# Performance work log

Measured on AMD Instinct MI355X. Metric: run time of the kernel, lower is better.

The kernel has to match this reference:

```python
import jax, jax.numpy as jnp
import numpy as np

N = 50000
E = 640000
NFEAT = 128
NHID = 128
ALPHA = 0.2  # leaky relu slope


def setup_inputs() -> dict:
    key = jax.random.key(0)
    k1, k2, k3, k4, k5 = jax.random.split(key, 5)
    x = jax.random.normal(k1, (N, NFEAT), dtype=jnp.float32)
    W = jax.random.normal(k2, (NFEAT, NHID), dtype=jnp.float32) * (1.0 / np.sqrt(NFEAT))
    a = jax.random.normal(k3, (1, 2 * NHID), dtype=jnp.float32) * 0.1
    # every node appears at least once as a source so rowsum > 0 (as in a real adjacency)
    src = jnp.concatenate([jnp.arange(N, dtype=jnp.int64 if jax.config.read('jax_enable_x64') else jnp.int32),
                           jax.random.randint(k4, (E - N,), 0, N)]).astype(jnp.int32)
    dst = jax.random.randint(k5, (E,), 0, N).astype(jnp.int32)
    edge_index = jnp.stack([src, dst], axis=0)
    return {"x": x, "W": W, "a": a, "edge_index": edge_index, "no_need_param": 0}


def reference(x, W, a, edge_index, no_need_param):
    # SpGraphAttentionLayer (concat=False), single head
    h = x @ W                                   # [N, nhid]
    src, dst = edge_index[0], edge_index[1]     # [E]
    nhid = W.shape[1]
    a1, a2 = a[0, :nhid], a[0, nhid:]
    # a @ cat(h[src], h[dst])  ==  h[src]@a1 + h[dst]@a2
    score = h[src] @ a1 + h[dst] @ a2           # [E]
    e = jnp.exp(-jax.nn.leaky_relu(score, ALPHA))
    n = x.shape[0]
    rowsum = jax.ops.segment_sum(e, src, num_segments=n)              # [N]
    h_prime = jax.ops.segment_sum(e[:, None] * h[dst], src, num_segments=n)  # [N, nhid]
    neighborhood_emb = h_prime / (rowsum[:, None] + 1e-16)
    # fused combine: elu(x @ W - neighborhood aggregation)
    mapped_fea = x @ W
    return jax.nn.elu(mapped_fea - neighborhood_emb)
```

## Files before the change

### kernel.cpp

```cpp
#include <hip/hip_runtime.h>
#include <hip/hip_fp16.h>
#include <math.h>

#define NFEAT 128
#define NHID  128
#define ALPHA 0.2f

typedef __attribute__((ext_vector_type(8))) short short8;
typedef __attribute__((ext_vector_type(4))) float f32x4;

__device__ inline unsigned int pack_bf16x2_rn(float x, float y) {
    unsigned int bx = __float_as_uint(x), by = __float_as_uint(y);
    bx += 0x7fffu + ((bx >> 16) & 1u);
    by += 0x7fffu + ((by >> 16) & 1u);
    return (bx >> 16) | (by & 0xffff0000u);
}

union Frag { unsigned int u[4]; uint4 v; short8 s; };

__global__ __launch_bounds__(256) void prep_wt_kernel(
    const float* __restrict__ W, unsigned int* __restrict__ Wtg)
{
    __shared__ float tile[32][33];
    const int t  = threadIdx.x;
    const int kt = blockIdx.x >> 2;
    const int nt = blockIdx.x & 3;

    {
        const int r = t >> 3, c = t & 7;
        const float4 v = *((const float4*)&W[(size_t)(kt * 32 + r) * NHID + nt * 32 + c * 4]);
        tile[r][c * 4 + 0] = v.x; tile[r][c * 4 + 1] = v.y;
        tile[r][c * 4 + 2] = v.z; tile[r][c * 4 + 3] = v.w;
    }
    __syncthreads();

    const int nn = t & 31;
    #pragma unroll
    for (int i = 0; i < 2; ++i) {
        const int kk = (t >> 5) * 2 + i;
        Wtg[(size_t)(nt * 32 + nn) * 64 + kt * 16 + kk] =
            pack_bf16x2_rn(tile[kk * 2][nn], tile[kk * 2 + 1][nn]);
    }
}

__global__ __launch_bounds__(256) void gemm_h_kernel(
    const float* __restrict__ x, const unsigned int* __restrict__ Wtg,
    const float* __restrict__ a, float* __restrict__ h,
    unsigned int* __restrict__ hbu,
    float* __restrict__ s1, float* __restrict__ s2, int n,
    const int* __restrict__ ei, int* __restrict__ hist, int E)
{
    __shared__ unsigned int Wtu[128 * 68];

    const int t = threadIdx.x;

    #pragma unroll
    for (int i = 0; i < 8; ++i) {
        const int u  = i * 256 + t;
        const uint4 v = ((const uint4*)Wtg)[u];
        const int nn = u >> 4, kc = u & 15;
        *((uint4*)&Wtu[nn * 68 + kc * 4]) = v;
    }

    {
        const int E4   = E >> 2;
        const int nthr = gridDim.x << 8;
        const int g    = blockIdx.x * 256 + t;
        for (int idx = g; idx < E4; idx += nthr) {
            const int4 s4 = ((const int4*)ei)[idx];
            atomicAdd(&hist[s4.x], 1);
            atomicAdd(&hist[s4.y], 1);
            atomicAdd(&hist[s4.z], 1);
            atomicAdd(&hist[s4.w], 1);
        }
        for (int j = (E4 << 2) + g; j < E; j += nthr) atomicAdd(&hist[ei[j]], 1);
    }
    __syncthreads();

    const int w    = t >> 6;
    const int lane = t & 63;
    const int c    = lane & 15;
    const int quad = lane >> 4;

    const int rowbase = blockIdx.x * 128 + w * 32;

    float a1v[8], a2v[8];
    #pragma unroll
    for (int tt = 0; tt < 8; ++tt) {
        a1v[tt] = a[tt * 16 + c];
        a2v[tt] = a[NHID + tt * 16 + c];
    }

    f32x4 acc[2][8];
    #pragma unroll
    for (int rt = 0; rt < 2; ++rt)
        #pragma unroll
        for (int tt = 0; tt < 8; ++tt)
            acc[rt][tt] = (f32x4){0.f, 0.f, 0.f, 0.f};

    #pragma unroll
    for (int s = 0; s < 4; ++s) {
        Frag afr[2];
        #pragma unroll
        for (int rt = 0; rt < 2; ++rt) {
            int row = rowbase + rt * 16 + c;
            if (row >= n) row = n - 1;
            const float* xp = x + (size_t)row * NFEAT + s * 32 + quad * 8;
            const float4 xa = *((const float4*)xp);
            const float4 xb = *((const float4*)(xp + 4));
            afr[rt].u[0] = pack_bf16x2_rn(xa.x, xa.y);
            afr[rt].u[1] = pack_bf16x2_rn(xa.z, xa.w);
            afr[rt].u[2] = pack_bf16x2_rn(xb.x, xb.y);
            afr[rt].u[3] = pack_bf16x2_rn(xb.z, xb.w);
        }
        #pragma unroll
        for (int tt = 0; tt < 8; ++tt) {
            Frag bfr;
            bfr.v = *((const uint4*)&Wtu[(tt * 16 + c) * 68 + s * 16 + quad * 4]);
            acc[0][tt] = __builtin_amdgcn_mfma_f32_16x16x32_bf16(
                afr[0].s, bfr.s, acc[0][tt], 0, 0, 0);
            acc[1][tt] = __builtin_amdgcn_mfma_f32_16x16x32_bf16(
                afr[1].s, bfr.s, acc[1][tt], 0, 0, 0);
        }
    }

    #pragma unroll
    for (int rt = 0; rt < 2; ++rt) {
        #pragma unroll
        for (int r = 0; r < 4; ++r) {
            const int  row = rowbase + rt * 16 + quad * 4 + r;
            const bool ok  = (row < n);
            float p1 = 0.f, p2 = 0.f;
            #pragma unroll
            for (int tt = 0; tt < 8; ++tt) {
                const float v = acc[rt][tt][r];
                if (ok) h[(size_t)row * NHID + tt * 16 + c] = v;
                p1 = fmaf(v, a1v[tt], p1);
                p2 = fmaf(v, a2v[tt], p2);
            }
            #pragma unroll
            for (int p = 0; p < 4; ++p) {
                if (ok) hbu[(size_t)row * 64 + p * 16 + c] =
                    pack_bf16x2_rn(acc[rt][2 * p][r], acc[rt][2 * p + 1][r]);
            }
            #pragma unroll
            for (int off = 1; off <= 8; off <<= 1) {
                p1 += __shfl_xor(p1, off, 64);
                p2 += __shfl_xor(p2, off, 64);
            }
            if (ok && c == 0) { s1[row] = p1; s2[row] = p2; }
        }
    }
}

__global__ __launch_bounds__(256) void scan_block_kernel(
    const int* __restrict__ in, int* __restrict__ out, int* __restrict__ bsums, int n)
{
    __shared__ int s[256];
    const int tid = threadIdx.x;
    const int gid = blockIdx.x * 256 + tid;
    const int v = (gid < n) ? in[gid] : 0;
    s[tid] = v;
    __syncthreads();
    #pragma unroll
    for (int off = 1; off < 256; off <<= 1) {
        const int t2 = (tid >= off) ? s[tid - off] : 0;
        __syncthreads();
        s[tid] += t2;
        __syncthreads();
    }
    if (gid < n) out[gid] = s[tid] - v;
    if (tid == 255 && bsums) bsums[blockIdx.x] = s[255];
}

__global__ __launch_bounds__(256) void scan_add_kernel(
    int* __restrict__ row_ptr, int* __restrict__ cursor,
    const int* __restrict__ bsums_scan, int n, int E)
{
    const int gid = blockIdx.x * 256 + threadIdx.x;
    if (gid < n) {
        const int v = row_ptr[gid] + bsums_scan[gid >> 8];
        row_ptr[gid] = v;
        cursor[gid]  = v;
    }
    if (gid == 0) row_ptr[n] = E;
}

__global__ __launch_bounds__(256) void scatter_kernel(
    const int* __restrict__ ei, const float* __restrict__ s1,
    const float* __restrict__ s2, int* __restrict__ cursor,
    unsigned int* __restrict__ erec, int E)
{
    const int j = blockIdx.x * 256 + threadIdx.x;
    if (j >= E) return;
    const int src = ei[j];
    const int dst = ei[E + j];
    float s = s1[src] + s2[dst];
    s = (s > 0.f) ? s : ALPHA * s;
    const float ev = expf(-s);
    const unsigned int evh = (unsigned int)__half_as_ushort(__float2half(ev));
    const int pos = atomicAdd(&cursor[src], 1);
    erec[pos] = ((unsigned int)dst << 16) | evh;
}

__global__ __launch_bounds__(256) void aggregate_kernel(
    const int* __restrict__ row_ptr, const unsigned int* __restrict__ erec,
    const unsigned int* __restrict__ hbu, const float* __restrict__ h,
    float* __restrict__ out, int n)
{
    const int node = blockIdx.x * 16 + (threadIdx.x >> 4);
    const int l    = threadIdx.x & 15;
    if (node >= n) return;

    const int beg = row_ptr[node];
    const int end = row_ptr[node + 1];

    float acc[8];
    #pragma unroll
    for (int i = 0; i < 8; ++i) acc[i] = 0.f;
    float rs = 0.f;

    #define BL(x) __uint_as_float((x) << 16)
    #define BH(x) __uint_as_float((x) & 0xffff0000u)
    #define ACC4(u, ev)                                   \
        acc[0] = fmaf(ev, BL(u.x), acc[0]);               \
        acc[4] = fmaf(ev, BH(u.x), acc[4]);               \
        acc[1] = fmaf(ev, BL(u.y), acc[1]);               \
        acc[5] = fmaf(ev, BH(u.y), acc[5]);               \
        acc[2] = fmaf(ev, BL(u.z), acc[2]);               \
        acc[6] = fmaf(ev, BH(u.z), acc[6]);               \
        acc[3] = fmaf(ev, BL(u.w), acc[3]);               \
        acc[7] = fmaf(ev, BH(u.w), acc[7]);

    int e = beg;
    for (; e + 8 <= end; e += 8) {
        unsigned int rr[8];
        uint4 u[8];
        #pragma unroll
        for (int i = 0; i < 8; ++i) rr[i] = erec[e + i];
        #pragma unroll
        for (int i = 0; i < 8; ++i)
            u[i] = ((const uint4*)(hbu + (size_t)(rr[i] >> 16) * 64))[l];
        #pragma unroll
        for (int i = 0; i < 8; ++i) {
            const float ev = __half2float(__ushort_as_half((unsigned short)(rr[i] & 0xffffu)));
            ACC4(u[i], ev);
            rs += ev;
        }
    }
    for (; e + 2 <= end; e += 2) {
        const unsigned int r0 = erec[e], r1 = erec[e + 1];
        const uint4 u0 = ((const uint4*)(hbu + (size_t)(r0 >> 16) * 64))[l];
        const uint4 u1 = ((const uint4*)(hbu + (size_t)(r1 >> 16) * 64))[l];
        const float e0 = __half2float(__ushort_as_half((unsigned short)(r0 & 0xffffu)));
        const float e1 = __half2float(__ushort_as_half((unsigned short)(r1 & 0xffffu)));
        ACC4(u0, e0); ACC4(u1, e1);
        rs += e0 + e1;
    }
    if (e < end) {
        const unsigned int r0 = erec[e];
        const uint4 u0 = ((const uint4*)(hbu + (size_t)(r0 >> 16) * 64))[l];
        const float e0 = __half2float(__ushort_as_half((unsigned short)(r0 & 0xffffu)));
        ACC4(u0, e0);
        rs += e0;
    }
    #undef ACC4
    #undef BL
    #undef BH

    const float rinv = 1.0f / (rs + 1e-16f);
    const int p = l >> 2, q = l & 3;
    const float4* hp4 = (const float4*)(h + (size_t)node * NHID);
    const float4 ha = hp4[8 * p + q];
    const float4 hb = hp4[8 * p + 4 + q];
    float4 oa, ob;
    float z;
    z = ha.x - acc[0] * rinv; oa.x = (z > 0.f) ? z : (expf(z) - 1.f);
    z = ha.y - acc[1] * rinv; oa.y = (z > 0.f) ? z : (expf(z) - 1.f);
    z = ha.z - acc[2] * rinv; oa.z = (z > 0.f) ? z : (expf(z) - 1.f);
    z = ha.w - acc[3] * rinv; oa.w = (z > 0.f) ? z : (expf(z) - 1.f);
    z = hb.x - acc[4] * rinv; ob.x = (z > 0.f) ? z : (expf(z) - 1.f);
    z = hb.y - acc[5] * rinv; ob.y = (z > 0.f) ? z : (expf(z) - 1.f);
    z = hb.z - acc[6] * rinv; ob.z = (z > 0.f) ? z : (expf(z) - 1.f);
    z = hb.w - acc[7] * rinv; ob.w = (z > 0.f) ? z : (expf(z) - 1.f);
    float4* op = (float4*)(out + (size_t)node * NHID);
    op[8 * p + q]     = oa;
    op[8 * p + 4 + q] = ob;
}

extern "C" void kernel_launch(void* const* d_in, const int* in_sizes, int n_in,
                              void* d_out, int out_size, void* d_ws, size_t ws_size,
                              hipStream_t stream) {
    const float* x  = (const float*)d_in[0];
    const float* W  = (const float*)d_in[1];
    const float* a  = (const float*)d_in[2];
    const int*   ei = (const int*)d_in[3];

    const int n = in_sizes[0] / NFEAT;
    const int E = in_sizes[3] / 2;
    const int nb = (n + 255) / 256;

    float* out = (float*)d_out;

    float*        h     = (float*)d_ws;
    unsigned int* hbu   = (unsigned int*)(h + (size_t)n * NHID);
    float*        s1    = (float*)(hbu + (size_t)n * 64);
    float*        s2    = s1 + n;
    unsigned int* erec  = (unsigned int*)(s2 + n);
    unsigned int* Wtg   = erec + E;
    int*          hist  = (int*)(Wtg + 8192);
    int*          bsums = hist + n;
    int*          bsums_scan = bsums + 256;
    int*          row_ptr    = bsums_scan + 256;
    int*          cursor     = row_ptr + (n + 1);

    hipMemsetAsync(hist, 0, ((size_t)n + 256) * sizeof(int), stream);

    prep_wt_kernel<<<16, 256, 0, stream>>>(W, Wtg);

    gemm_h_kernel<<<(n + 127) / 128, 256, 0, stream>>>(x, Wtg, a, h, hbu, s1, s2, n,
                                                       ei, hist, E);

    scan_block_kernel<<<nb, 256, 0, stream>>>(hist, row_ptr, bsums, n);
    scan_block_kernel<<<1, 256, 0, stream>>>(bsums, bsums_scan, nullptr, 256);
    scan_add_kernel<<<nb, 256, 0, stream>>>(row_ptr, cursor, bsums_scan, n, E);

    scatter_kernel<<<(E + 255) / 256, 256, 0, stream>>>(ei, s1, s2, cursor, erec, E);

    aggregate_kernel<<<(n + 15) / 16, 256, 0, stream>>>(row_ptr, erec, hbu, h, out, n);
}
```

Before: 191.8 us.

## Split histogram into dedicated blocks and shrink GEMM tile with swizzled LDS

```diff
diff --git a/kernel.cpp b/kernel.cpp
--- a/kernel.cpp
+++ b/kernel.cpp
@@ -48,24 +48,16 @@
     const float* __restrict__ a, float* __restrict__ h,
     unsigned int* __restrict__ hbu,
     float* __restrict__ s1, float* __restrict__ s2, int n,
-    const int* __restrict__ ei, int* __restrict__ hist, int E)
-{
-    __shared__ unsigned int Wtu[128 * 68];
+    const int* __restrict__ ei, int* __restrict__ hist, int E, int gemm_blocks)
+{
+    __shared__ unsigned int Wtu[128 * 64];
 
     const int t = threadIdx.x;
 
-    #pragma unroll
-    for (int i = 0; i < 8; ++i) {
-        const int u  = i * 256 + t;
-        const uint4 v = ((const uint4*)Wtg)[u];
-        const int nn = u >> 4, kc = u & 15;
-        *((uint4*)&Wtu[nn * 68 + kc * 4]) = v;
-    }
-
-    {
+    if (blockIdx.x >= gemm_blocks) {
         const int E4   = E >> 2;
-        const int nthr = gridDim.x << 8;
-        const int g    = blockIdx.x * 256 + t;
+        const int nthr = (gridDim.x - gemm_blocks) << 8;
+        const int g    = (blockIdx.x - gemm_blocks) * 256 + t;
         for (int idx = g; idx < E4; idx += nthr) {
             const int4 s4 = ((const int4*)ei)[idx];
             atomicAdd(&hist[s4.x], 1);
@@ -74,15 +66,32 @@
             atomicAdd(&hist[s4.w], 1);
         }
         for (int j = (E4 << 2) + g; j < E; j += nthr) atomicAdd(&hist[ei[j]], 1);
-    }
-    __syncthreads();
+        return;
+    }
+
+    #pragma unroll
+    for (int i = 0; i < 8; ++i) {
+        const int u  = i * 256 + t;
+        const uint4 v = ((const uint4*)Wtg)[u];
+        const int nn = u >> 4, kc = u & 15;
+        *((uint4*)&Wtu[nn * 64 + (kc ^ (nn & 15)) * 4]) = v;
+    }
 
     const int w    = t >> 6;
     const int lane = t & 63;
     const int c    = lane & 15;
     const int quad = lane >> 4;
 
-    const int rowbase = blockIdx.x * 128 + w * 32;
+    const int rowbase = blockIdx.x * 64 + w * 16;
+
+    int arow = rowbase + c; if (arow >= n) arow = n - 1;
+    const float4* xp = (const float4*)(x + (size_t)arow * NFEAT);
+    float4 xv[8];
+    #pragma unroll
+    for (int s = 0; s < 4; ++s) {
+        xv[2 * s]     = xp[s * 8 + quad * 2];
+        xv[2 * s + 1] = xp[s * 8 + quad * 2 + 1];
+    }
 
     float a1v[8], a2v[8];
     #pragma unroll
@@ -91,65 +100,52 @@
         a2v[tt] = a[NHID + tt * 16 + c];
     }
 
-    f32x4 acc[2][8];
-    #pragma unroll
-    for (int rt = 0; rt < 2; ++rt)
-        #pragma unroll
-        for (int tt = 0; tt < 8; ++tt)
-            acc[rt][tt] = (f32x4){0.f, 0.f, 0.f, 0.f};
+    f32x4 acc[8];
+    #pragma unroll
+    for (int tt = 0; tt < 8; ++tt) acc[tt] = (f32x4){0.f, 0.f, 0.f, 0.f};
+
+    __syncthreads();
 
     #pragma unroll
     for (int s = 0; s < 4; ++s) {
-        Frag afr[2];
-        #pragma unroll
-        for (int rt = 0; rt < 2; ++rt) {
-            int row = rowbase + rt * 16 + c;
-            if (row >= n) row = n - 1;
-            const float* xp = x + (size_t)row * NFEAT + s * 32 + quad * 8;
-            const float4 xa = *((const float4*)xp);
-            const float4 xb = *((const float4*)(xp + 4));
-            afr[rt].u[0] = pack_bf16x2_rn(xa.x, xa.y);
-            afr[rt].u[1] = pack_bf16x2_rn(xa.z, xa.w);
-            afr[rt].u[2] = pack_bf16x2_rn(xb.x, xb.y);
-            afr[rt].u[3] = pack_bf16x2_rn(xb.z, xb.w);
-        }
+        Frag afr;
+        afr.u[0] = pack_bf16x2_rn(xv[2 * s].x,     xv[2 * s].y);
+        afr.u[1] = pack_bf16x2_rn(xv[2 * s].z,     xv[2 * s].w);
+        afr.u[2] = pack_bf16x2_rn(xv[2 * s + 1].x, xv[2 * s + 1].y);
+        afr.u[3] = pack_bf16x2_rn(xv[2 * s + 1].z, xv[2 * s + 1].w);
+        const int kc = s * 4 + quad;
         #pragma unroll
         for (int tt = 0; tt < 8; ++tt) {
             Frag bfr;
-            bfr.v = *((const uint4*)&Wtu[(tt * 16 + c) * 68 + s * 16 + quad * 4]);
-            acc[0][tt] = __builtin_amdgcn_mfma_f32_16x16x32_bf16(
-                afr[0].s, bfr.s, acc[0][tt], 0, 0, 0);
-            acc[1][tt] = __builtin_amdgcn_mfma_f32_16x16x32_bf16(
-                afr[1].s, bfr.s, acc[1][tt], 0, 0, 0);
-        }
-    }
-
-    #pragma unroll
-    for (int rt = 0; rt < 2; ++rt) {
-        #pragma unroll
-        for (int r = 0; r < 4; ++r) {
-            const int  row = rowbase + rt * 16 + quad * 4 + r;
-            const bool ok  = (row < n);
-            float p1 = 0.f, p2 = 0.f;
-            #pragma unroll
-            for (int tt = 0; tt < 8; ++tt) {
-                const float v = acc[rt][tt][r];
-                if (ok) h[(size_t)row * NHID + tt * 16 + c] = v;
-                p1 = fmaf(v, a1v[tt], p1);
-                p2 = fmaf(v, a2v[tt], p2);
-            }
-            #pragma unroll
-            for (int p = 0; p < 4; ++p) {
-                if (ok) hbu[(size_t)row * 64 + p * 16 + c] =
-                    pack_bf16x2_rn(acc[rt][2 * p][r], acc[rt][2 * p + 1][r]);
-            }
-            #pragma unroll
-            for (int off = 1; off <= 8; off <<= 1) {
-                p1 += __shfl_xor(p1, off, 64);
-                p2 += __shfl_xor(p2, off, 64);
-            }
-            if (ok && c == 0) { s1[row] = p1; s2[row] = p2; }
-        }
+            bfr.v = *((const uint4*)&Wtu[(tt * 16 + c) * 64 + (kc ^ c) * 4]);
+            acc[tt] = __builtin_amdgcn_mfma_f32_16x16x32_bf16(
+                afr.s, bfr.s, acc[tt], 0, 0, 0);
+        }
+    }
+
+    #pragma unroll
+    for (int r = 0; r < 4; ++r) {
+        const int  row = rowbase + quad * 4 + r;
+        const bool ok  = (row < n);
+        float p1 = 0.f, p2 = 0.f;
+        #pragma unroll
+        for (int tt = 0; tt < 8; ++tt) {
+            const float v = acc[tt][r];
+            if (ok) h[(size_t)row * NHID + tt * 16 + c] = v;
+            p1 = fmaf(v, a1v[tt], p1);
+            p2 = fmaf(v, a2v[tt], p2);
+        }
+        #pragma unroll
+        for (int p = 0; p < 4; ++p) {
+            if (ok) hbu[(size_t)row * 64 + p * 16 + c] =
+                pack_bf16x2_rn(acc[2 * p][r], acc[2 * p + 1][r]);
+        }
+        #pragma unroll
+        for (int off = 1; off <= 8; off <<= 1) {
+            p1 += __shfl_xor(p1, off, 64);
+            p2 += __shfl_xor(p2, off, 64);
+        }
+        if (ok && c == 0) { s1[row] = p1; s2[row] = p2; }
     }
 }
 
@@ -318,8 +314,10 @@
 
     prep_wt_kernel<<<16, 256, 0, stream>>>(W, Wtg);
 
-    gemm_h_kernel<<<(n + 127) / 128, 256, 0, stream>>>(x, Wtg, a, h, hbu, s1, s2, n,
-                                                       ei, hist, E);
+    const int gemm_blocks = (n + 63) / 64;
+    const int hist_blocks = 128;
+    gemm_h_kernel<<<gemm_blocks + hist_blocks, 256, 0, stream>>>(
+        x, Wtg, a, h, hbu, s1, s2, n, ei, hist, E, gemm_blocks);
 
     scan_block_kernel<<<nb, 256, 0, stream>>>(hist, row_ptr, bsums, n);
     scan_block_kernel<<<1, 256, 0, stream>>>(bsums, bsums_scan, nullptr, 256);
```

New measurement: 180.6 us. 5.9% less time.
